# Optimization experiments

Hardware: AMD Instinct MI355X
Metric: run time of the kernel (lower is better)

The kernel has to match this reference:

```python
import jax, jax.numpy as jnp
import numpy as np

NUM_ENT = 14541
NUM_REL = 474
D = 400
B = 32
N_CAND = 14505


def setup_inputs() -> dict:
    key = jax.random.key(0)
    k0, k1, k2, k4, k5 = jax.random.split(key, 5)
    return {
        "arg0_1": jax.random.normal(k0, (NUM_ENT, D), dtype=jnp.float32),   # entity embeddings
        "arg1_1": jax.random.normal(k1, (NUM_REL, D), dtype=jnp.float32),   # relation centers
        "arg2_1": jax.random.uniform(k2, (NUM_REL, D), dtype=jnp.float32),  # relation offsets (box widths)
        "arg3_1": jnp.ones((1,), dtype=jnp.float32),                        # margin gamma
        "arg4_1": jax.random.randint(k4, (B, 2), 0, NUM_REL),               # (head_id, rel_id) pairs
        "arg5_1": jax.random.randint(k5, (4, N_CAND), 0, NUM_ENT),          # candidate entity ids (row 0 used)
    }


def reference(arg0_1, arg1_1, arg2_1, arg3_1, arg4_1, arg5_1):
    # Gather heads / relation params
    head = arg0_1[arg4_1[:, 0]]            # [B, D]
    rel_c = arg1_1[arg4_1[:, 1]]           # [B, D]
    rel_o = arg2_1[arg4_1[:, 1]]           # [B, D]

    query = (head + rel_c)[:, None, :]     # [B, 1, D] box center
    offset = rel_o[:, None, :]             # [B, 1, D] box width

    # Candidate tail embeddings: only row 0 of arg5_1 is used in the graph
    cand = arg0_1[arg5_1[0].reshape(-1)][None, :, :]  # [1, N_CAND, D]

    d = jnp.abs(cand - query)                           # [B, N_CAND, D]
    dist_outside = jax.nn.relu(d - offset).sum(-1)      # [B, N_CAND]
    dist_inside = jnp.abs(jnp.minimum(d, offset)).sum(-1)

    return arg3_1 - dist_outside - 0.02 * dist_inside   # [B, N_CAND]
```

## Files before the change

kernel.cpp:

```cpp
#include <hip/hip_runtime.h>

#define DIM     400
#define B       32
#define NCAND   14505
#define NROUND  3627
#define TSTRIPS 256
#define THREADS 256

__global__ __launch_bounds__(THREADS, 2)
void score_kernel(const float* __restrict__ ent,
                  const float* __restrict__ relc,
                  const float* __restrict__ relo,
                  const float* __restrict__ onev,
                  const int*   __restrict__ pairs,
                  const int*   __restrict__ cidx,
                  float* __restrict__ out) {
    const int fid  = blockIdx.x;
    const int xcd  = fid & 7;
    const int rest = fid >> 3;
    const int bq   = rest & 7;
    const int tc   = rest >> 3;
    const int t    = xcd + 8 * tc;

    const int tid  = threadIdx.x;
    const int lane = tid & 63;
    const int u    = lane & 15;
    const int g    = lane >> 4;
    const int b    = __builtin_amdgcn_readfirstlane(bq * 4 + (tid >> 6));

    const int hd = pairs[b * 2 + 0];
    const int rl = pairs[b * 2 + 1];
    const float* hbase = ent  + (size_t)hd * DIM + u;
    const float* cbase = relc + (size_t)rl * DIM + u;
    const float* obase = relo + (size_t)rl * DIM + u;

    float q[25], o[25];
    float oa = 0.f;
#pragma unroll
    for (int k = 0; k < 25; ++k) {
        q[k] = hbase[16 * k] + cbase[16 * k];
        o[k] = obase[16 * k];
        oa  += o[k];
    }
    oa += __shfl_xor(oa, 1);
    oa += __shfl_xor(oa, 2);
    oa += __shfl_xor(oa, 4);
    oa += __shfl_xor(oa, 8);
    const float base = onev[0] + 0.98f * oa;

    const float* entu = ent + u;

    auto rowp = [&](int rr) -> const float* {
        int cand = 4 * rr + g;
        int ci   = cidx[cand < NCAND ? cand : NCAND - 1];
        return entu + (size_t)ci * DIM;
    };

#define LOADROW(buf, rr)                                   \
    {                                                      \
        const float* p_ = rowp(rr);                        \
        _Pragma("unroll")                                  \
        for (int k = 0; k < 25; ++k) buf[k] = p_[16 * k];  \
    }

#define COMPSTORE(buf, rr)                                         \
    {                                                              \
        float am = 0.f, ad = 0.f;                                  \
        _Pragma("unroll")                                          \
        for (int k = 0; k < 25; ++k) {                             \
            float d_ = buf[k] - q[k];                              \
            float a_ = fabsf(d_);                                  \
            am += fmaxf(a_, o[k]);                                 \
            ad += a_;                                              \
        }                                                          \
        float s_ = fmaf(-0.98f, am, -0.02f * ad);                  \
        s_ += __shfl_xor(s_, 1);                                   \
        s_ += __shfl_xor(s_, 2);                                   \
        s_ += __shfl_xor(s_, 4);                                   \
        s_ += __shfl_xor(s_, 8);                                   \
        const int cand_ = 4 * (rr) + g;                            \
        if (u == 0 && cand_ < NCAND)                               \
            out[(size_t)b * NCAND + cand_] = base + s_;            \
    }

    float bufA[25], bufB[25];
    LOADROW(bufA, t)
    for (int rr = t; rr < NROUND; rr += 2 * TSTRIPS) {
        LOADROW(bufB, rr + TSTRIPS)
        COMPSTORE(bufA, rr)
        LOADROW(bufA, rr + 2 * TSTRIPS)
        if (rr + TSTRIPS < NROUND)
            COMPSTORE(bufB, rr + TSTRIPS)
    }
#undef LOADROW
#undef COMPSTORE
}

extern "C" void kernel_launch(void* const* d_in, const int* in_sizes, int n_in,
                              void* d_out, int out_size, void* d_ws, size_t ws_size,
                              hipStream_t stream) {
    const float* ent   = (const float*)d_in[0];
    const float* relc  = (const float*)d_in[1];
    const float* relo  = (const float*)d_in[2];
    const float* onev  = (const float*)d_in[3];
    const int*   pairs = (const int*)d_in[4];
    const int*   cidx  = (const int*)d_in[5];
    float*       out   = (float*)d_out;

    const int grid = 8 * 8 * 32;
    score_kernel<<<grid, THREADS, 0, stream>>>(ent, relc, relo, onev, pairs, cidx, out);
}
```

Measured before the change: 44.85 us.

## Vectorize candidate row loads to float4 and drop manual double buffering

Each 16-lane group now loads a 400-float row as 100 float4s: six strided float4 loads per lane, plus a seventh on the first four lanes. This replaces 25 scalar loads per lane and cuts the number of memory instructions. The explicit two-buffer software pipeline is removed in favour of a simple loop with two accumulator pairs, leaving overlap of loads across rows to the compiler and to wave occupancy. The row work is now uneven across lanes, and without the prefetch the next row's gather latency may no longer be hidden.

```diff
diff --git a/kernel.cpp b/kernel.cpp
--- a/kernel.cpp
+++ b/kernel.cpp
@@ -30,17 +30,24 @@
 
     const int hd = pairs[b * 2 + 0];
     const int rl = pairs[b * 2 + 1];
-    const float* hbase = ent  + (size_t)hd * DIM + u;
-    const float* cbase = relc + (size_t)rl * DIM + u;
-    const float* obase = relo + (size_t)rl * DIM + u;
+    const float4* hb = (const float4*)(ent  + (size_t)hd * DIM) + u;
+    const float4* cb = (const float4*)(relc + (size_t)rl * DIM) + u;
+    const float4* ob = (const float4*)(relo + (size_t)rl * DIM) + u;
 
-    float q[25], o[25];
+    float4 q[7], o[7];
     float oa = 0.f;
 #pragma unroll
-    for (int k = 0; k < 25; ++k) {
-        q[k] = hbase[16 * k] + cbase[16 * k];
-        o[k] = obase[16 * k];
-        oa  += o[k];
+    for (int k = 0; k < 6; ++k) {
+        float4 h = hb[16 * k], c = cb[16 * k];
+        q[k] = make_float4(h.x + c.x, h.y + c.y, h.z + c.z, h.w + c.w);
+        o[k] = ob[16 * k];
+        oa += o[k].x + o[k].y + o[k].z + o[k].w;
+    }
+    if (u < 4) {
+        float4 h = hb[96], c = cb[96];
+        q[6] = make_float4(h.x + c.x, h.y + c.y, h.z + c.z, h.w + c.w);
+        o[6] = ob[96];
+        oa += o[6].x + o[6].y + o[6].z + o[6].w;
     }
     oa += __shfl_xor(oa, 1);
     oa += __shfl_xor(oa, 2);
@@ -48,52 +55,47 @@
     oa += __shfl_xor(oa, 8);
     const float base = onev[0] + 0.98f * oa;
 
-    const float* entu = ent + u;
+    const float4* entu = (const float4*)ent + u;
 
-    auto rowp = [&](int rr) -> const float* {
-        int cand = 4 * rr + g;
-        int ci   = cidx[cand < NCAND ? cand : NCAND - 1];
-        return entu + (size_t)ci * DIM;
-    };
+    for (int rr = t; rr < NROUND; rr += TSTRIPS) {
+        const int cand = 4 * rr + g;
+        const int ci   = cidx[cand < NCAND ? cand : NCAND - 1];
+        const float4* p = entu + (size_t)ci * 100;
 
-#define LOADROW(buf, rr)                                   \
-    {                                                      \
-        const float* p_ = rowp(rr);                        \
-        _Pragma("unroll")                                  \
-        for (int k = 0; k < 25; ++k) buf[k] = p_[16 * k];  \
+        float4 cbuf[7];
+#pragma unroll
+        for (int k = 0; k < 6; ++k) cbuf[k] = p[16 * k];
+        if (u < 4) cbuf[6] = p[96];
+
+        float am0 = 0.f, ad0 = 0.f, am1 = 0.f, ad1 = 0.f;
+#define E(vc, vq, vo, AM, AD)                     \
+        {                                         \
+            float d_ = (vc) - (vq);               \
+            AM += fmaxf(fabsf(d_), (vo));         \
+            AD += fabsf(d_);                      \
+        }
+#define F4(k, AM, AD)                             \
+        E(cbuf[k].x, q[k].x, o[k].x, AM, AD)      \
+        E(cbuf[k].y, q[k].y, o[k].y, AM, AD)      \
+        E(cbuf[k].z, q[k].z, o[k].z, AM, AD)      \
+        E(cbuf[k].w, q[k].w, o[k].w, AM, AD)
+
+        F4(0, am0, ad0) F4(1, am1, ad1)
+        F4(2, am0, ad0) F4(3, am1, ad1)
+        F4(4, am0, ad0) F4(5, am1, ad1)
+        if (u < 4) { F4(6, am0, ad0) }
+#undef F4
+#undef E
+
+        float s_ = fmaf(-0.98f, am0 + am1, -0.02f * (ad0 + ad1));
+        s_ += __shfl_xor(s_, 1);
+        s_ += __shfl_xor(s_, 2);
+        s_ += __shfl_xor(s_, 4);
+        s_ += __shfl_xor(s_, 8);
+
+        if (u == 0 && cand < NCAND)
+            out[(size_t)b * NCAND + cand] = base + s_;
     }
-
-#define COMPSTORE(buf, rr)                                         \
-    {                                                              \
-        float am = 0.f, ad = 0.f;                                  \
-        _Pragma("unroll")                                          \
-        for (int k = 0; k < 25; ++k) {                             \
-            float d_ = buf[k] - q[k];                              \
-            float a_ = fabsf(d_);                                  \
-            am += fmaxf(a_, o[k]);                                 \
-            ad += a_;                                              \
-        }                                                          \
-        float s_ = fmaf(-0.98f, am, -0.02f * ad);                  \
-        s_ += __shfl_xor(s_, 1);                                   \
-        s_ += __shfl_xor(s_, 2);                                   \
-        s_ += __shfl_xor(s_, 4);                                   \
-        s_ += __shfl_xor(s_, 8);                                   \
-        const int cand_ = 4 * (rr) + g;                            \
-        if (u == 0 && cand_ < NCAND)                               \
-            out[(size_t)b * NCAND + cand_] = base + s_;            \
-    }
-
-    float bufA[25], bufB[25];
-    LOADROW(bufA, t)
-    for (int rr = t; rr < NROUND; rr += 2 * TSTRIPS) {
-        LOADROW(bufB, rr + TSTRIPS)
-        COMPSTORE(bufA, rr)
-        LOADROW(bufA, rr + 2 * TSTRIPS)
-        if (rr + TSTRIPS < NROUND)
-            COMPSTORE(bufB, rr + TSTRIPS)
-    }
-#undef LOADROW
-#undef COMPSTORE
 }
 
 extern "C" void kernel_launch(void* const* d_in, const int* in_sizes, int n_in,
```

After: 46.16 us. 2.9% more time.
